# Kernel tuning notes

Measured on AMD Instinct MI355X. Metric: run time of the kernel, lower is better.

Reference implementation:

```python
import jax, jax.numpy as jnp
import numpy as np
from jax import lax

T = 512
CHUNK = 64
H = W = 28
C = 4
D_MODEL = H * W * C  # 3136
D_HIDDEN = 512
ALPHA = 0.9
ETA0 = 0.1
P = 2.0
EPS = 1e-6


def setup_inputs() -> dict:
    key = jax.random.key(0)
    ks = jax.random.split(key, 8)
    x = jax.random.normal(ks[0], (T, C, H, W), dtype=jnp.float32)
    conv_k_w = jax.random.normal(ks[1], (3, 3, C, C), dtype=jnp.float32) / 6.0  # lecun-ish: fan_in=36
    conv_v_w = jax.random.normal(ks[2], (3, 3, C, C), dtype=jnp.float32) / 6.0
    conv_k_b = jnp.zeros((C,), jnp.float32)
    conv_v_b = jnp.zeros((C,), jnp.float32)
    rms_k_scale = jnp.ones((C,), jnp.float32)
    rms_v_scale = jnp.ones((C,), jnp.float32)
    W1 = jax.random.normal(ks[3], (D_MODEL, D_HIDDEN), dtype=jnp.float32) / np.sqrt(D_MODEL).astype(np.float32)
    b1 = jnp.zeros((D_HIDDEN,), jnp.float32)
    W2 = jax.random.normal(ks[4], (D_HIDDEN, D_MODEL), dtype=jnp.float32) / np.sqrt(D_HIDDEN).astype(np.float32)
    b2 = jnp.zeros((D_MODEL,), jnp.float32)
    return {"x": x, "conv_k_w": conv_k_w, "conv_k_b": conv_k_b,
            "conv_v_w": conv_v_w, "conv_v_b": conv_v_b,
            "rms_k_scale": rms_k_scale, "rms_v_scale": rms_v_scale,
            "W1": W1, "b1": b1, "W2": W2, "b2": b2}


def _conv(x_nhwc, w, b):
    y = lax.conv_general_dilated(x_nhwc, w, window_strides=(1, 1), padding='SAME',
                                 dimension_numbers=('NHWC', 'HWIO', 'NHWC'))
    return y + b


def _rmsnorm(z, scale):
    inv = lax.rsqrt(jnp.mean(z * z, axis=-1, keepdims=True) + EPS)
    return z * inv * scale


def _mlp(params, k):
    w1, bb1, w2, bb2 = params
    return jax.nn.gelu(k @ w1 + bb1) @ w2 + bb2


def reference(x, conv_k_w, conv_k_b, conv_v_w, conv_v_b, rms_k_scale, rms_v_scale, W1, b1, W2, b2):
    t = x.shape[0]
    xh = jnp.transpose(x, (0, 2, 3, 1))  # [T,H,W,C]
    nk = _rmsnorm(_conv(xh, conv_k_w, conv_k_b), rms_k_scale).reshape(t, -1)  # [T, D_MODEL]
    nv = _rmsnorm(_conv(xh, conv_v_w, conv_v_b), rms_v_scale).reshape(t, -1)

    params0 = (W1, b1, W2, b2)

    def loss_per_token(params, k, v):
        pred = _mlp(params, k)
        return jnp.sum(jnp.abs(pred - v) ** P)

    etas = ETA0 * ALPHA ** jnp.arange(CHUNK, dtype=jnp.float32)
    betas = ALPHA ** jnp.arange(CHUNK, dtype=jnp.float32)
    weights = etas * (betas[-1] / betas)  # [CHUNK]

    n_chunks = t // CHUNK
    Kc = nk.reshape(n_chunks, CHUNK, D_MODEL)
    Vc = nv.reshape(n_chunks, CHUNK, D_MODEL)

    def chunk_body(params, kv):
        K, V = kv
        # per-token parameter grads: leaves have leading CHUNK axis
        grads = jax.vmap(jax.grad(loss_per_token), in_axes=(None, 0, 0))(params, K, V)
        new_params = jax.tree.map(
            lambda p, g: p - jnp.tensordot(weights, g, axes=((0,), (0,))), params, grads)
        Y = _mlp(new_params, K)  # recall on keys with updated fast weights
        return new_params, Y

    _, Y_chunks = lax.scan(chunk_body, params0, (Kc, Vc))
    Y = Y_chunks.reshape(t, D_MODEL)
    return Y.reshape(t, C, H, W)
```

## Files before the change

kernel.cpp:

```cpp
#include <hip/hip_runtime.h>
#include <math.h>

#define DM 3136
#define DH 512

typedef __attribute__((ext_vector_type(8))) short bf16x8;
typedef __attribute__((ext_vector_type(4))) float f32x4;

__device__ __forceinline__ ushort f2bf(float f) {
  union { float f; unsigned u; } v; v.f = f;
  unsigned r = v.u + 0x7FFFu + ((v.u >> 16) & 1u);
  return (ushort)(r >> 16);
}

#define MICRO_4x4 \
    acc[0][0] += a.x*b.x; acc[0][1] += a.x*b.y; acc[0][2] += a.x*b.z; acc[0][3] += a.x*b.w; \
    acc[1][0] += a.y*b.x; acc[1][1] += a.y*b.y; acc[1][2] += a.y*b.z; acc[1][3] += a.y*b.w; \
    acc[2][0] += a.z*b.x; acc[2][1] += a.z*b.y; acc[2][2] += a.z*b.z; acc[2][3] += a.z*b.w; \
    acc[3][0] += a.w*b.x; acc[3][1] += a.w*b.y; acc[3][2] += a.w*b.z; acc[3][3] += a.w*b.w;

__device__ __forceinline__ void gelu_both(float xx, float& g, float& gp) {
  const float c = 0.7978845608028654f;
  const float a = 0.044715f;
  float x2 = xx * xx;
  float u = c * (xx + a * xx * x2);
  float t = tanhf(u);
  g  = 0.5f * xx * (1.f + t);
  gp = 0.5f * (1.f + t) + 0.5f * xx * (1.f - t * t) * c * (1.f + 3.f * a * x2);
}
__device__ __forceinline__ float gelu_only(float xx) {
  const float c = 0.7978845608028654f;
  const float a = 0.044715f;
  float u = c * (xx + a * xx * xx * xx);
  return 0.5f * xx * (1.f + tanhf(u));
}

__device__ __forceinline__ void nt64_core(
    const ushort* __restrict__ A, int lda,
    const ushort* __restrict__ B, int ldb,
    int ksteps, f32x4* acc) {
  int lane = threadIdx.x & 63;
  int wv = threadIdx.x >> 6;
  int qr = wv >> 1, qc = wv & 1;
  int lr = lane & 15;
  int lk = (lane >> 4) << 3;
  const ushort* pa0 = A + (size_t)(qr * 32 + lr) * lda + lk;
  const ushort* pa1 = pa0 + (size_t)16 * lda;
  const ushort* pb0 = B + (size_t)(qc * 32 + lr) * ldb + lk;
  const ushort* pb1 = pb0 + (size_t)16 * ldb;
  bf16x8 a0 = *(const bf16x8*)pa0;
  bf16x8 a1 = *(const bf16x8*)pa1;
  bf16x8 b0 = *(const bf16x8*)pb0;
  bf16x8 b1 = *(const bf16x8*)pb1;
  for (int s = 0; s < ksteps; ++s) {
    int sn = (s + 1 < ksteps) ? (s + 1) * 32 : s * 32;
    bf16x8 na0 = *(const bf16x8*)(pa0 + sn);
    bf16x8 na1 = *(const bf16x8*)(pa1 + sn);
    bf16x8 nb0 = *(const bf16x8*)(pb0 + sn);
    bf16x8 nb1 = *(const bf16x8*)(pb1 + sn);
    acc[0] = __builtin_amdgcn_mfma_f32_16x16x32_bf16(a0, b0, acc[0], 0, 0, 0);
    acc[1] = __builtin_amdgcn_mfma_f32_16x16x32_bf16(a0, b1, acc[1], 0, 0, 0);
    acc[2] = __builtin_amdgcn_mfma_f32_16x16x32_bf16(a1, b0, acc[2], 0, 0, 0);
    acc[3] = __builtin_amdgcn_mfma_f32_16x16x32_bf16(a1, b1, acc[3], 0, 0, 0);
    a0 = na0; a1 = na1; b0 = nb0; b1 = nb1;
  }
}

__device__ __forceinline__ void nt64_store(const f32x4* acc, float* __restrict__ dst, int ldc) {
  int lane = threadIdx.x & 63, wv = threadIdx.x >> 6;
  int r0 = (wv >> 1) * 32 + ((lane >> 4) << 2);
  int c0 = (wv & 1) * 32 + (lane & 15);
  #pragma unroll
  for (int r = 0; r < 4; ++r) {
    dst[(size_t)(r0 + r) * ldc + c0]           = acc[0][r];
    dst[(size_t)(r0 + r) * ldc + c0 + 16]      = acc[1][r];
    dst[(size_t)(r0 + r + 16) * ldc + c0]      = acc[2][r];
    dst[(size_t)(r0 + r + 16) * ldc + c0 + 16] = acc[3][r];
  }
}

__global__ __launch_bounds__(256) void conv_rms(
    const float* __restrict__ x,
    const float* __restrict__ wk, const float* __restrict__ bk,
    const float* __restrict__ wv, const float* __restrict__ bv,
    const float* __restrict__ sk, const float* __restrict__ sv,
    const float* __restrict__ W1, ushort* __restrict__ w1tb,
    const float* __restrict__ W2, ushort* __restrict__ W2b0, ushort* __restrict__ W2tb0,
    ushort* __restrict__ nkb, float* __restrict__ nv) {
  __shared__ float smem[4160];
  int tid = threadIdx.x;
  if (blockIdx.x >= 1960) {
    int t = blockIdx.x - 1960;
    int d0 = (t % 49) * 64, h0 = (t / 49) * 64;
    int c = tid & 63, rq = tid >> 6;
    #pragma unroll
    for (int q = 0; q < 16; ++q) {
      int r = q * 4 + rq;
      float v = W2[(size_t)(h0 + r) * DM + d0 + c];
      smem[r * 65 + c] = v;
      W2b0[(size_t)(h0 + r) * DM + d0 + c] = f2bf(v);
    }
    __syncthreads();
    #pragma unroll
    for (int q = 0; q < 16; ++q) {
      int r = q * 4 + rq;
      W2tb0[(size_t)(d0 + r) * DH + h0 + c] = f2bf(smem[c * 65 + r]);
    }
    return;
  }
  if (blockIdx.x >= 1568) {
    int t = blockIdx.x - 1568;
    int d0 = (t % 49) * 64, h0 = (t / 49) * 64;
    int c = tid & 63, rq = tid >> 6;
    #pragma unroll
    for (int q = 0; q < 16; ++q) {
      int r = q * 4 + rq;
      smem[r * 65 + c] = W1[(size_t)(d0 + r) * 512 + h0 + c];
    }
    __syncthreads();
    #pragma unroll
    for (int q = 0; q < 16; ++q) {
      int r = q * 4 + rq;
      w1tb[(size_t)(h0 + r) * 3136 + d0 + c] = f2bf(smem[c * 65 + r]);
    }
    return;
  }
  float* swk = smem;
  float* swv = smem + 144;
  float* sb  = smem + 288;
  if (tid < 144) { swk[tid] = wk[tid]; swv[tid] = wv[tid]; }
  if (tid < 4) {
    sb[tid] = bk[tid]; sb[4 + tid] = bv[tid];
    sb[8 + tid] = sk[tid]; sb[12 + tid] = sv[tid];
  }
  __syncthreads();
  int idx = blockIdx.x * 256 + tid;
  int t = idx / 784, hw = idx - t * 784;
  int h = hw / 28, w = hw - h * 28;
  float ak[4], av[4];
  #pragma unroll
  for (int c = 0; c < 4; ++c) { ak[c] = sb[c]; av[c] = sb[4 + c]; }
  const float* xt = x + (size_t)t * DM;
  for (int kh = 0; kh < 3; ++kh) {
    int ih = h + kh - 1;
    if (ih < 0 || ih >= 28) continue;
    for (int kw = 0; kw < 3; ++kw) {
      int iw = w + kw - 1;
      if (iw < 0 || iw >= 28) continue;
      int base = (kh * 3 + kw) * 16;
      #pragma unroll
      for (int ci = 0; ci < 4; ++ci) {
        float xv = xt[ci * 784 + ih * 28 + iw];
        #pragma unroll
        for (int co = 0; co < 4; ++co) {
          ak[co] += xv * swk[base + ci * 4 + co];
          av[co] += xv * swv[base + ci * 4 + co];
        }
      }
    }
  }
  float mk = (ak[0]*ak[0] + ak[1]*ak[1] + ak[2]*ak[2] + ak[3]*ak[3]) * 0.25f + 1e-6f;
  float mv = (av[0]*av[0] + av[1]*av[1] + av[2]*av[2] + av[3]*av[3]) * 0.25f + 1e-6f;
  float ik = 1.f / sqrtf(mk), iv = 1.f / sqrtf(mv);
  ushort4 ok = { f2bf(ak[0]*ik*sb[8]), f2bf(ak[1]*ik*sb[9]),
                 f2bf(ak[2]*ik*sb[10]), f2bf(ak[3]*ik*sb[11]) };
  float4 ov = { av[0]*iv*sb[12], av[1]*iv*sb[13], av[2]*iv*sb[14], av[3]*iv*sb[15] };
  *(ushort4*)&nkb[(size_t)idx * 4] = ok;
  *(float4*)&nv[(size_t)idx * 4] = ov;
}

__global__ __launch_bounds__(256) void u1_kernel(
    const ushort* __restrict__ nkb, const ushort* __restrict__ w1tb,
    float* __restrict__ KKsl, float* __restrict__ Hb_sl) {
  f32x4 acc[4] = {{0.f,0.f,0.f,0.f},{0.f,0.f,0.f,0.f},{0.f,0.f,0.f,0.f},{0.f,0.f,0.f,0.f}};
  int job = blockIdx.x;
  if (job < 448) {
    int s = job % 7;
    int t = job / 7;
    int m0 = (t >> 3) * 64, n0 = (t & 7) * 64;
    nt64_core(nkb + (size_t)m0 * DM + s * 448, DM, w1tb + (size_t)n0 * DM + s * 448, DM, 14, acc);
    nt64_store(acc, Hb_sl + (size_t)s * 262144 + (size_t)m0 * 512 + n0, 512);
  } else {
    int j2 = job - 448;
    int p = j2 / 7, s = j2 % 7;
    int c = 0;
    while ((c + 1) * (c + 2) / 2 <= p) ++c;
    int j = p - c * (c + 1) / 2;
    nt64_core(nkb + (size_t)c * 64 * DM + s * 448, DM, nkb + (size_t)j * 64 * DM + s * 448, DM, 14, acc);
    nt64_store(acc, KKsl + ((size_t)p * 7 + s) * 4096, 64);
  }
}

__global__ __launch_bounds__(256) void u2_kernel(
    const float* __restrict__ KKsl, const float* __restrict__ Hb_sl,
    float* __restrict__ KKf, float* __restrict__ Hbase,
    const float* __restrict__ b1,
    float* __restrict__ Hh, ushort* __restrict__ Gb, ushort* __restrict__ Gtb,
    float* __restrict__ Gp) {
  int i = blockIdx.x * 256 + threadIdx.x;
  if (i < 147456) {
    int pair = i >> 12, e = i & 4095;
    float s = 0.f;
    #pragma unroll
    for (int t = 0; t < 7; ++t) s += KKsl[((size_t)pair * 7 + t) * 4096 + e];
    KKf[i] = s;
  } else {
    int j = i - 147456;
    float s = 0.f;
    #pragma unroll
    for (int t = 0; t < 7; ++t) s += Hb_sl[(size_t)t * 262144 + j];
    Hbase[j] = s;
    if (j < 32768) {
      Hh[j] = s;
      float g, gp;
      gelu_both(s + b1[j & 511], g, gp);
      Gb[j] = f2bf(g);
      Gtb[(j & 511) * 64 + (j >> 9)] = f2bf(g);
      Gp[j] = gp;
    }
  }
}

__device__ __forceinline__ void hred_body(
    int j, const float* __restrict__ Hb_c, const float* __restrict__ Hcorr, int nsl,
    const float* __restrict__ b1v,
    float* __restrict__ Hh, ushort* __restrict__ Gb, ushort* __restrict__ Gtb,
    float* __restrict__ Gp) {
  float s = Hb_c[j];
  for (int t = 0; t < nsl; ++t) s -= Hcorr[(size_t)t * 32768 + j];
  Hh[j] = s;
  float g, gp;
  gelu_both(s + b1v[j & 511], g, gp);
  Gb[j] = f2bf(g);
  Gtb[(j & 511) * 64 + (j >> 9)] = f2bf(g);
  Gp[j] = gp;
}

__device__ __forceinline__ void hs_corr_job(
    const float* __restrict__ KK, const float* __restrict__ Ewj,
    float* __restrict__ dst, int bx, float* smem) {
  float* As = smem;
  float* Bs = smem + 4096;
  int tid = threadIdx.x;
  int n0 = bx * 64;
  {
    int m = tid >> 2, ib = (tid & 3) * 16;
    #pragma unroll
    for (int q = 0; q < 4; ++q) {
      float4 v = *(const float4*)(KK + m * 64 + ib + q * 4);
      As[(ib + q*4 + 0)*64 + m] = v.x;
      As[(ib + q*4 + 1)*64 + m] = v.y;
      As[(ib + q*4 + 2)*64 + m] = v.z;
      As[(ib + q*4 + 3)*64 + m] = v.w;
    }
    int kr = tid >> 4, nn = (tid & 15) * 4;
    #pragma unroll
    for (int q = 0; q < 4; ++q)
      *(float4*)&Bs[(kr + q*16)*64 + nn] = *(const float4*)(Ewj + (size_t)(kr + q*16) * DH + n0 + nn);
  }
  __syncthreads();
  int tx = tid & 15, ty = tid >> 4;
  float acc[4][4] = {{0.f}};
  #pragma unroll 16
  for (int kk = 0; kk < 64; ++kk) {
    float4 a = *(const float4*)&As[kk*64 + ty * 4];
    float4 b = *(const float4*)&Bs[kk*64 + tx * 4];
    MICRO_4x4
  }
  #pragma unroll
  for (int r = 0; r < 4; ++r) {
    float4 v = { acc[r][0], acc[r][1], acc[r][2], acc[r][3] };
    *(float4*)&dst[(ty*4 + r) * DH + n0 + tx*4] = v;
  }
}

__global__ __launch_bounds__(256) void p4w2_kernel(
    const ushort* __restrict__ Dwb, const ushort* __restrict__ Dwtb,
    const ushort* __restrict__ Gtb, const ushort* __restrict__ W2b_c,
    const float* __restrict__ W2c, float* __restrict__ W2n,
    ushort* __restrict__ W2b_n, ushort* __restrict__ W2tb_n,
    float* __restrict__ Esl) {
  f32x4 acc[4] = {{0.f,0.f,0.f,0.f},{0.f,0.f,0.f,0.f},{0.f,0.f,0.f,0.f},{0.f,0.f,0.f,0.f}};
  int b = blockIdx.x;
  if (b < 56) {
    int s = b % 7, nt = b / 7;
    nt64_core(Dwb + s * 448, DM, W2b_c + (size_t)nt * 64 * DM + s * 448, DM, 14, acc);
    nt64_store(acc, Esl + (size_t)s * 32768 + nt * 64, 512);
  } else {
    int li = b - 56;
    int d0 = (li % 49) * 64, h0 = (li / 49) * 64;
    nt64_core(Gtb + (size_t)h0 * 64, 64, Dwtb + (size_t)d0 * 64, 64, 2, acc);
    int lane = threadIdx.x & 63, wvv = threadIdx.x >> 6;
    int r0 = (wvv >> 1) * 32 + ((lane >> 4) << 2);
    int c0 = (wvv & 1) * 32 + (lane & 15);
    #pragma unroll
    for (int r = 0; r < 4; ++r) {
      #pragma unroll
      for (int p = 0; p < 4; ++p) {
        int h = h0 + r0 + r + ((p >> 1) ? 16 : 0);
        int d = d0 + c0 + ((p & 1) ? 16 : 0);
        size_t off = (size_t)h * DM + d;
        float w = W2c[off] - acc[p][r];
        W2n[off] = w;
        ushort wb = f2bf(w);
        W2b_n[off] = wb;
        W2tb_n[(size_t)d * DH + h] = wb;
      }
    }
  }
}

__global__ __launch_bounds__(256) void g2h_kernel(
    const float* __restrict__ KKf, int ch,
    const float* __restrict__ Esl, const float* __restrict__ GpC,
    const float* __restrict__ Hcur, const float* __restrict__ b1e,
    float* __restrict__ b1o, ushort* __restrict__ G2b,
    float* __restrict__ EwOut, float* __restrict__ Hcorr) {
  __shared__ float smem[8192];
  int blk = blockIdx.x;
  int tid = threadIdx.x;
  int tri = ch * (ch + 1) / 2;
  if (blk < 32) {
    float* KKs = smem;
    float* Ews = smem + 4096;
    float* b1l = smem + 5120;
    const float* KKcc = KKf + (size_t)(tri + ch) * 4096;
    int n0 = blk * 16;
    #pragma unroll
    for (int q = 0; q < 4; ++q) {
      int e4 = q * 256 + tid;
      *(float4*)&KKs[e4 * 4] = *(const float4*)(KKcc + e4 * 4);
    }
    #pragma unroll
    for (int q = 0; q < 4; ++q) {
      int e = q * 256 + tid;
      int i = e >> 4, cc = e & 15;
      size_t off = (size_t)i * 512 + n0 + cc;
      float s = 0.f;
      #pragma unroll
      for (int sl = 0; sl < 7; ++sl) s += Esl[(size_t)sl * 32768 + off];
      Ews[e] = s * GpC[off];
    }
    __syncthreads();
    if (tid < 16) {
      float s = 0.f;
      for (int i = 0; i < 64; ++i) s += Ews[i * 16 + tid];
      b1l[tid] = b1e[n0 + tid] - s;
    }
    __syncthreads();
    #pragma unroll
    for (int q = 0; q < 4; ++q) {
      int e = q * 256 + tid;
      int mrow = e >> 4, cc = e & 15;
      float corr = 0.f;
      #pragma unroll 16
      for (int i = 0; i < 64; ++i) corr += KKs[mrow * 64 + i] * Ews[i * 16 + cc];
      float xx = Hcur[(size_t)mrow * 512 + n0 + cc] - corr + b1l[cc];
      G2b[(size_t)mrow * 512 + n0 + cc] = f2bf(gelu_only(xx));
    }
  } else {
    float* As = smem;
    float* Bs = smem + 4096;
    int bx = blk - 32;
    int n0 = bx * 64;
    #pragma unroll
    for (int q = 0; q < 16; ++q) {
      int e = q * 256 + tid;
      int k = e >> 6, c = e & 63;
      size_t off = (size_t)k * 512 + n0 + c;
      float s = 0.f;
      #pragma unroll
      for (int sl = 0; sl < 7; ++sl) s += Esl[(size_t)sl * 32768 + off];
      float ew = s * GpC[off];
      Bs[k * 64 + c] = ew;
      EwOut[off] = ew;
    }
    {
      const float* KK = KKf + (size_t)((ch + 1) * (ch + 2) / 2 + ch) * 4096;
      int m = tid >> 2, ib = (tid & 3) * 16;
      #pragma unroll
      for (int q = 0; q < 4; ++q) {
        float4 v = *(const float4*)(KK + m * 64 + ib + q * 4);
        As[(ib + q*4 + 0)*64 + m] = v.x;
        As[(ib + q*4 + 1)*64 + m] = v.y;
        As[(ib + q*4 + 2)*64 + m] = v.z;
        As[(ib + q*4 + 3)*64 + m] = v.w;
      }
    }
    __syncthreads();
    if (tid < 64) {
      float s = 0.f;
      for (int k = 0; k < 64; ++k) s += Bs[k * 64 + tid];
      b1o[n0 + tid] = b1e[n0 + tid] - s;
    }
    int tx = tid & 15, ty = tid >> 4;
    float acc[4][4] = {{0.f}};
    #pragma unroll 16
    for (int kk = 0; kk < 64; ++kk) {
      float4 a = *(const float4*)&As[kk*64 + ty * 4];
      float4 b = *(const float4*)&Bs[kk*64 + tx * 4];
      MICRO_4x4
    }
    float* dst = Hcorr + (size_t)ch * 32768;
    #pragma unroll
    for (int r = 0; r < 4; ++r) {
      float4 v = { acc[r][0], acc[r][1], acc[r][2], acc[r][3] };
      *(float4*)&dst[(ty*4 + r) * DH + n0 + tx*4] = v;
    }
  }
}

__global__ __launch_bounds__(256) void p7h_kernel(
    const ushort* __restrict__ G2b, const ushort* __restrict__ W2tb,
    const float* __restrict__ b2n, float* __restrict__ out, int t0,
    const float* __restrict__ Hbase_n, const float* __restrict__ Hcorr, int nsl,
    const float* __restrict__ b1n,
    float* __restrict__ Hh, ushort* __restrict__ Gb_n, ushort* __restrict__ Gtb_n,
    float* __restrict__ Gp) {
  int b = blockIdx.x;
  if (b < 49) {
    f32x4 acc[4] = {{0.f,0.f,0.f,0.f},{0.f,0.f,0.f,0.f},{0.f,0.f,0.f,0.f},{0.f,0.f,0.f,0.f}};
    int n0 = b * 64;
    nt64_core(G2b, 512, W2tb + (size_t)n0 * 512, 512, 16, acc);
    int lane = threadIdx.x & 63, wvv = threadIdx.x >> 6;
    int r0 = (wvv >> 1) * 32 + ((lane >> 4) << 2);
    int c0 = (wvv & 1) * 32 + (lane & 15);
    #pragma unroll
    for (int r = 0; r < 4; ++r) {
      #pragma unroll
      for (int p = 0; p < 4; ++p) {
        int m = r0 + r + ((p >> 1) ? 16 : 0);
        int d = n0 + c0 + ((p & 1) ? 16 : 0);
        out[(size_t)(t0 + m) * DM + d] = acc[p][r] + b2n[d];
      }
    }
  } else {
    int j = (b - 49) * 256 + threadIdx.x;
    hred_body(j, Hbase_n, Hcorr, nsl, b1n, Hh, Gb_n, Gtb_n, Gp);
  }
}

__global__ __launch_bounds__(256) void p3d_kernel(
    const ushort* __restrict__ Gnb, const ushort* __restrict__ W2tb,
    const float* __restrict__ Vn, const float* __restrict__ b2in, float wc2,
    float* __restrict__ b2out, ushort* __restrict__ Dwb, ushort* __restrict__ Dwtb,
    const float* __restrict__ KKf, int ch,
    const float* __restrict__ Ewst, float* __restrict__ Hcorr) {
  __shared__ float smem[8192];
  int blk = blockIdx.x;
  if (blk < 49) {
    f32x4 acc[4] = {{0.f,0.f,0.f,0.f},{0.f,0.f,0.f,0.f},{0.f,0.f,0.f,0.f},{0.f,0.f,0.f,0.f}};
    int n0 = blk * 64;
    nt64_core(Gnb, 512, W2tb + (size_t)n0 * 512, 512, 16, acc);
    int lane = threadIdx.x & 63, wvv = threadIdx.x >> 6;
    int qr = wvv >> 1, qc = wvv & 1;
    int r0 = qr * 32 + ((lane >> 4) << 2);
    int c0 = qc * 32 + (lane & 15);
    float csum[2] = {0.f, 0.f};
    #pragma unroll
    for (int r = 0; r < 4; ++r) {
      #pragma unroll
      for (int p = 0; p < 4; ++p) {
        int m = r0 + r + ((p >> 1) ? 16 : 0);
        int dl = c0 + ((p & 1) ? 16 : 0);
        int d = n0 + dl;
        float dw = wc2 * (acc[p][r] + b2in[d] - Vn[(size_t)m * DM + d]);
        ushort db = f2bf(dw);
        Dwb[(size_t)m * DM + d] = db;
        Dwtb[(size_t)d * 64 + m] = db;
        csum[p & 1] += dw;
      }
    }
    int slot = qr * 4 + ((lane >> 4) & 3);
    smem[(size_t)c0 * 8 + slot] = csum[0];
    smem[(size_t)(c0 + 16) * 8 + slot] = csum[1];
    __syncthreads();
    if (threadIdx.x < 64) {
      float s = 0.f;
      #pragma unroll
      for (int q = 0; q < 8; ++q) s += smem[threadIdx.x * 8 + q];
      b2out[n0 + threadIdx.x] = b2in[n0 + threadIdx.x] - s;
    }
  } else {
    int j2 = blk - 49;
    int j = j2 >> 3, bx = j2 & 7;
    int trin = (ch + 2) * (ch + 3) / 2;
    hs_corr_job(KKf + (size_t)(trin + j) * 4096, Ewst + (size_t)j * 32768,
                Hcorr + (size_t)j * 32768, bx, smem);
  }
}

extern "C" void kernel_launch(void* const* d_in, const int* in_sizes, int n_in,
                              void* d_out, int out_size, void* d_ws, size_t ws_size,
                              hipStream_t stream) {
  const float* x  = (const float*)d_in[0];
  const float* wk = (const float*)d_in[1];
  const float* bk = (const float*)d_in[2];
  const float* wv = (const float*)d_in[3];
  const float* bv = (const float*)d_in[4];
  const float* sk = (const float*)d_in[5];
  const float* sv = (const float*)d_in[6];
  const float* W1 = (const float*)d_in[7];
  const float* b1 = (const float*)d_in[8];
  const float* W2 = (const float*)d_in[9];
  const float* b2 = (const float*)d_in[10];
  float* out = (float*)d_out;
  float* ws  = (float*)d_ws;

  ushort* nkb   = (ushort*)ws;
  ushort* w1tb  = (ushort*)(ws + 802816);
  float* nv     = ws + 1605632;
  float* W2A    = nv + 1605632;
  float* W2B    = W2A + 1605632;
  float* bf_base = W2B + 1605632;
  ushort* W2b0  = (ushort*)bf_base;
  ushort* W2tb0 = (ushort*)(bf_base + 802816);
  ushort* W2bA  = (ushort*)(bf_base + 1605632);
  ushort* W2bB  = (ushort*)(bf_base + 2408448);
  ushort* W2tbA = (ushort*)(bf_base + 3211264);
  ushort* W2tbB = (ushort*)(bf_base + 4014080);
  float* Esl    = bf_base + 4816896;
  float* Hb_sl  = Esl + 229376;
  float* KKsl   = Hb_sl + 1835008;
  float* Hbase  = KKsl + 1032192;
  float* KKf    = Hbase + 262144;
  float* HhA    = KKf + 147456;
  float* HhB    = HhA + 32768;
  float* GpA    = HhB + 32768;
  float* GpB    = GpA + 32768;
  ushort* GbA   = (ushort*)(GpB + 32768);
  ushort* GbB   = (ushort*)(GpB + 49152);
  ushort* GtbA  = (ushort*)(GpB + 65536);
  ushort* GtbB  = (ushort*)(GpB + 81920);
  ushort* G2b   = (ushort*)(GpB + 98304);
  ushort* Dwb   = (ushort*)(GpB + 114688);
  ushort* Dwtb  = (ushort*)(GpB + 215040);
  float* Ewst   = GpB + 315392;
  float* Hcorr  = Ewst + 262144;
  float* b1A    = Hcorr + 229376;
  float* b1B    = b1A + 512;
  float* b2A    = b1B + 512;
  float* b2B    = b2A + 3136;

  float* W2buf[2]   = { W2A, W2B };
  ushort* W2bb[2]   = { W2bA, W2bB };
  ushort* W2tbb[2]  = { W2tbA, W2tbB };
  ushort* Gbb[2]    = { GbA, GbB };
  ushort* Gtbb[2]   = { GtbA, GtbB };
  float* Hhb[2]     = { HhA, HhB };
  float* Gpb[2]     = { GpA, GpB };
  float* b1buf[2]   = { b1A, b1B };
  float* b2buf[2]   = { b2A, b2B };

  float wc2 = 2.0f * (float)(0.1 * pow(0.9, 63.0));

  conv_rms<<<2352, 256, 0, stream>>>(x, wk, bk, wv, bv, sk, sv,
                                     W1, w1tb, W2, W2b0, W2tb0, nkb, nv);
  u1_kernel<<<700, 256, 0, stream>>>(nkb, w1tb, KKsl, Hb_sl);
  u2_kernel<<<1600, 256, 0, stream>>>(KKsl, Hb_sl, KKf, Hbase, b1, HhA, GbA, GtbA, GpA);
  p3d_kernel<<<49, 256, 0, stream>>>(GbA, W2tb0, nv, b2, wc2, b2A, Dwb, Dwtb,
                                     KKf, 0, Ewst, Hcorr);

  for (int ch = 0; ch < 8; ++ch) {
    const float* b1e  = ch ? b1buf[(ch - 1) & 1] : b1;
    const float* W2c  = ch ? W2buf[(ch - 1) & 1] : W2;
    const ushort* W2b_c = ch ? W2bb[(ch - 1) & 1] : W2b0;

    p4w2_kernel<<<448, 256, 0, stream>>>(
        Dwb, Dwtb, Gtbb[ch & 1], W2b_c, W2c,
        W2buf[ch & 1], W2bb[ch & 1], W2tbb[ch & 1], Esl);
    g2h_kernel<<<32 + (ch < 7 ? 8 : 0), 256, 0, stream>>>(
        KKf, ch, Esl, Gpb[ch & 1], Hhb[ch & 1], b1e, b1buf[ch & 1],
        G2b, Ewst + (size_t)ch * 32768, Hcorr);
    p7h_kernel<<<49 + (ch < 7 ? 128 : 0), 256, 0, stream>>>(
        G2b, W2tbb[ch & 1], b2buf[ch & 1], out, ch * 64,
        Hbase + (size_t)((ch + 1) & 7) * 32768, Hcorr, ch + 1, b1buf[ch & 1],
        Hhb[(ch + 1) & 1], Gbb[(ch + 1) & 1], Gtbb[(ch + 1) & 1], Gpb[(ch + 1) & 1]);
    if (ch < 7) {
      int gF = 49 + (ch < 6 ? 8 * (ch + 1) : 0);
      p3d_kernel<<<gF, 256, 0, stream>>>(
          Gbb[(ch + 1) & 1], W2tbb[ch & 1], nv + (size_t)(ch + 1) * 200704,
          b2buf[ch & 1], wc2, b2buf[(ch + 1) & 1], Dwb, Dwtb,
          KKf, ch, Ewst, Hcorr);
    }
  }
}
```

Baseline: 418.2 us.

## Replace explicit W2 updates with low-rank correction terms against the original W2

Stops materializing the updated W2 matrix (fp32 plus two bf16 copies) every chunk. W2 is now kept implicitly as the original W2 minus a sum of low-rank G^T·Dw products, and all Dw and G histories are stored. Predictions and error backprop are rebuilt from the original W2 plus small 64x64 Gram-style corrections (DD, -G·G^T). The per-chunk kernels are regrouped into four stages, and the hidden-state recompute is folded into the g2h-like kernel. The goal is to remove the large 512x3136 read-modify-write per chunk, at the cost of correction work that grows with the chunk index and extra rounding from bf16 correction matrices.

```diff
diff --git a/kernel.cpp b/kernel.cpp
--- a/kernel.cpp
+++ b/kernel.cpp
@@ -11,6 +11,10 @@
   union { float f; unsigned u; } v; v.f = f;
   unsigned r = v.u + 0x7FFFu + ((v.u >> 16) & 1u);
   return (ushort)(r >> 16);
+}
+__device__ __forceinline__ float bf2f(ushort u) {
+  union { float f; unsigned u; } v; v.u = ((unsigned)u) << 16;
+  return v.f;
 }
 
 #define MICRO_4x4 \
@@ -79,6 +83,57 @@
   }
 }
 
+__device__ __forceinline__ void store_neg_gg(const f32x4* acc, ushort* __restrict__ dst) {
+  int lane = threadIdx.x & 63, wv = threadIdx.x >> 6;
+  int r0 = (wv >> 1) * 32 + ((lane >> 4) << 2);
+  int c0 = (wv & 1) * 32 + (lane & 15);
+  #pragma unroll
+  for (int r = 0; r < 4; ++r) {
+    #pragma unroll
+    for (int p = 0; p < 4; ++p) {
+      int m = r0 + r + ((p >> 1) ? 16 : 0);
+      int n = c0 + ((p & 1) ? 16 : 0);
+      dst[m * 64 + n] = f2bf(-acc[p][r]);
+    }
+  }
+}
+
+__device__ __forceinline__ void dw_epilogue(
+    const f32x4* acc, int n0, const float* __restrict__ Vn,
+    const float* __restrict__ b2in, float wc2,
+    ushort* __restrict__ Dwb_o, ushort* __restrict__ Dwt_o,
+    float* __restrict__ b2out, float* smem) {
+  int lane = threadIdx.x & 63, wvv = threadIdx.x >> 6;
+  int qr = wvv >> 1, qc = wvv & 1;
+  int r0 = qr * 32 + ((lane >> 4) << 2);
+  int c0 = qc * 32 + (lane & 15);
+  float csum[2] = {0.f, 0.f};
+  #pragma unroll
+  for (int r = 0; r < 4; ++r) {
+    #pragma unroll
+    for (int p = 0; p < 4; ++p) {
+      int m = r0 + r + ((p >> 1) ? 16 : 0);
+      int dl = c0 + ((p & 1) ? 16 : 0);
+      int d = n0 + dl;
+      float dw = wc2 * (acc[p][r] + b2in[d] - Vn[(size_t)m * DM + d]);
+      ushort db = f2bf(dw);
+      Dwb_o[(size_t)m * DM + d] = db;
+      Dwt_o[(size_t)d * 64 + m] = db;
+      csum[p & 1] += dw;
+    }
+  }
+  int slot = qr * 4 + ((lane >> 4) & 3);
+  smem[(size_t)c0 * 8 + slot] = csum[0];
+  smem[(size_t)(c0 + 16) * 8 + slot] = csum[1];
+  __syncthreads();
+  if (threadIdx.x < 64) {
+    float s = 0.f;
+    #pragma unroll
+    for (int q = 0; q < 8; ++q) s += smem[threadIdx.x * 8 + q];
+    b2out[n0 + threadIdx.x] = b2in[n0 + threadIdx.x] - s;
+  }
+}
+
 __global__ __launch_bounds__(256) void conv_rms(
     const float* __restrict__ x,
     const float* __restrict__ wk, const float* __restrict__ bk,
@@ -221,21 +276,6 @@
   }
 }
 
-__device__ __forceinline__ void hred_body(
-    int j, const float* __restrict__ Hb_c, const float* __restrict__ Hcorr, int nsl,
-    const float* __restrict__ b1v,
-    float* __restrict__ Hh, ushort* __restrict__ Gb, ushort* __restrict__ Gtb,
-    float* __restrict__ Gp) {
-  float s = Hb_c[j];
-  for (int t = 0; t < nsl; ++t) s -= Hcorr[(size_t)t * 32768 + j];
-  Hh[j] = s;
-  float g, gp;
-  gelu_both(s + b1v[j & 511], g, gp);
-  Gb[j] = f2bf(g);
-  Gtb[(j & 511) * 64 + (j >> 9)] = f2bf(g);
-  Gp[j] = gp;
-}
-
 __device__ __forceinline__ void hs_corr_job(
     const float* __restrict__ KK, const float* __restrict__ Ewj,
     float* __restrict__ dst, int bx, float* smem) {
@@ -274,154 +314,176 @@
   }
 }
 
-__global__ __launch_bounds__(256) void p4w2_kernel(
-    const ushort* __restrict__ Dwb, const ushort* __restrict__ Dwtb,
-    const ushort* __restrict__ Gtb, const ushort* __restrict__ W2b_c,
-    const float* __restrict__ W2c, float* __restrict__ W2n,
-    ushort* __restrict__ W2b_n, ushort* __restrict__ W2tb_n,
-    float* __restrict__ Esl) {
+__global__ __launch_bounds__(256) void pred0_kernel(
+    const ushort* __restrict__ Gb0, const ushort* __restrict__ W2tb0,
+    const float* __restrict__ V, const float* __restrict__ b2in, float wc2,
+    float* __restrict__ b2out, ushort* __restrict__ Dwb_o, ushort* __restrict__ Dwt_o) {
+  __shared__ float smem[512];
+  f32x4 acc[4] = {{0.f,0.f,0.f,0.f},{0.f,0.f,0.f,0.f},{0.f,0.f,0.f,0.f},{0.f,0.f,0.f,0.f}};
+  int n0 = blockIdx.x * 64;
+  nt64_core(Gb0, 512, W2tb0 + (size_t)n0 * 512, 512, 16, acc);
+  dw_epilogue(acc, n0, V, b2in, wc2, Dwb_o, Dwt_o, b2out, smem);
+}
+
+__global__ __launch_bounds__(256) void kA_kernel(
+    const ushort* __restrict__ Dwb_ch, const ushort* __restrict__ W2b0,
+    const ushort* __restrict__ Dwb_all, float* __restrict__ Esl,
+    float* __restrict__ DD) {
   f32x4 acc[4] = {{0.f,0.f,0.f,0.f},{0.f,0.f,0.f,0.f},{0.f,0.f,0.f,0.f},{0.f,0.f,0.f,0.f}};
   int b = blockIdx.x;
   if (b < 56) {
     int s = b % 7, nt = b / 7;
-    nt64_core(Dwb + s * 448, DM, W2b_c + (size_t)nt * 64 * DM + s * 448, DM, 14, acc);
+    nt64_core(Dwb_ch + s * 448, DM, W2b0 + (size_t)nt * 64 * DM + s * 448, DM, 14, acc);
     nt64_store(acc, Esl + (size_t)s * 32768 + nt * 64, 512);
   } else {
-    int li = b - 56;
-    int d0 = (li % 49) * 64, h0 = (li / 49) * 64;
-    nt64_core(Gtb + (size_t)h0 * 64, 64, Dwtb + (size_t)d0 * 64, 64, 2, acc);
-    int lane = threadIdx.x & 63, wvv = threadIdx.x >> 6;
-    int r0 = (wvv >> 1) * 32 + ((lane >> 4) << 2);
-    int c0 = (wvv & 1) * 32 + (lane & 15);
-    #pragma unroll
-    for (int r = 0; r < 4; ++r) {
+    int j = b - 56;
+    nt64_core(Dwb_ch, DM, Dwb_all + (size_t)j * 200704, DM, 98, acc);
+    nt64_store(acc, DD + (size_t)j * 4096, 64);
+  }
+}
+
+__global__ __launch_bounds__(256) void kB_kernel(
+    const float* __restrict__ KKf, int ch,
+    const float* __restrict__ Esl, const float* __restrict__ DD,
+    const ushort* __restrict__ Gtb_all, const float* __restrict__ GpC,
+    const float* __restrict__ Hcur, const float* __restrict__ b1e,
+    float* __restrict__ b1o, ushort* __restrict__ G2b, float* __restrict__ EwOut,
+    const float* __restrict__ Hcorr, const float* __restrict__ Hbase_n,
+    float* __restrict__ HhN, ushort* __restrict__ GbN,
+    ushort* __restrict__ GtbN, float* __restrict__ GpN) {
+  __shared__ float sKK[4096];
+  __shared__ float sKK2[4096];
+  __shared__ float sDD[4096];
+  __shared__ float sG[1024];
+  __shared__ float sEw[1024];
+  __shared__ float b1l[16];
+  int tid = threadIdx.x;
+  int n0 = blockIdx.x * 16;
+  int tri = ch * (ch + 1) / 2;
+  {
+    const float* KKcc = KKf + (size_t)(tri + ch) * 4096;
+    #pragma unroll
+    for (int q = 0; q < 4; ++q)
+      ((float4*)sKK)[q * 256 + tid] = ((const float4*)KKcc)[q * 256 + tid];
+    if (ch < 7) {
+      const float* KKn = KKf + (size_t)((ch + 1) * (ch + 2) / 2 + ch) * 4096;
       #pragma unroll
-      for (int p = 0; p < 4; ++p) {
-        int h = h0 + r0 + r + ((p >> 1) ? 16 : 0);
-        int d = d0 + c0 + ((p & 1) ? 16 : 0);
-        size_t off = (size_t)h * DM + d;
-        float w = W2c[off] - acc[p][r];
-        W2n[off] = w;
-        ushort wb = f2bf(w);
-        W2b_n[off] = wb;
-        W2tb_n[(size_t)d * DH + h] = wb;
-      }
-    }
-  }
-}
-
-__global__ __launch_bounds__(256) void g2h_kernel(
-    const float* __restrict__ KKf, int ch,
-    const float* __restrict__ Esl, const float* __restrict__ GpC,
-    const float* __restrict__ Hcur, const float* __restrict__ b1e,
-    float* __restrict__ b1o, ushort* __restrict__ G2b,
-    float* __restrict__ EwOut, float* __restrict__ Hcorr) {
-  __shared__ float smem[8192];
-  int blk = blockIdx.x;
-  int tid = threadIdx.x;
-  int tri = ch * (ch + 1) / 2;
-  if (blk < 32) {
-    float* KKs = smem;
-    float* Ews = smem + 4096;
-    float* b1l = smem + 5120;
-    const float* KKcc = KKf + (size_t)(tri + ch) * 4096;
-    int n0 = blk * 16;
-    #pragma unroll
-    for (int q = 0; q < 4; ++q) {
-      int e4 = q * 256 + tid;
-      *(float4*)&KKs[e4 * 4] = *(const float4*)(KKcc + e4 * 4);
-    }
+      for (int q = 0; q < 4; ++q)
+        ((float4*)sKK2)[q * 256 + tid] = ((const float4*)KKn)[q * 256 + tid];
+    }
+  }
+  float eDel[4] = {0.f, 0.f, 0.f, 0.f};
+  for (int j = 0; j < ch; ++j) {
+    __syncthreads();
+    const float* DDj = DD + (size_t)j * 4096;
+    #pragma unroll
+    for (int q = 0; q < 4; ++q)
+      ((float4*)sDD)[q * 256 + tid] = ((const float4*)DDj)[q * 256 + tid];
+    const ushort* Gt = Gtb_all + (size_t)j * 32768 + (size_t)n0 * 64;
     #pragma unroll
     for (int q = 0; q < 4; ++q) {
       int e = q * 256 + tid;
-      int i = e >> 4, cc = e & 15;
-      size_t off = (size_t)i * 512 + n0 + cc;
-      float s = 0.f;
-      #pragma unroll
-      for (int sl = 0; sl < 7; ++sl) s += Esl[(size_t)sl * 32768 + off];
-      Ews[e] = s * GpC[off];
-    }
-    __syncthreads();
-    if (tid < 16) {
-      float s = 0.f;
-      for (int i = 0; i < 64; ++i) s += Ews[i * 16 + tid];
-      b1l[tid] = b1e[n0 + tid] - s;
+      sG[e] = bf2f(Gt[e]);
     }
     __syncthreads();
     #pragma unroll
     for (int q = 0; q < 4; ++q) {
       int e = q * 256 + tid;
-      int mrow = e >> 4, cc = e & 15;
-      float corr = 0.f;
+      int m = e >> 4, c = e & 15;
+      float s = 0.f;
       #pragma unroll 16
-      for (int i = 0; i < 64; ++i) corr += KKs[mrow * 64 + i] * Ews[i * 16 + cc];
-      float xx = Hcur[(size_t)mrow * 512 + n0 + cc] - corr + b1l[cc];
-      G2b[(size_t)mrow * 512 + n0 + cc] = f2bf(gelu_only(xx));
-    }
+      for (int n = 0; n < 64; ++n) s += sDD[m * 64 + n] * sG[c * 64 + n];
+      eDel[q] += s;
+    }
+  }
+  __syncthreads();
+  #pragma unroll
+  for (int q = 0; q < 4; ++q) {
+    int e = q * 256 + tid;
+    int m = e >> 4, c = e & 15;
+    size_t off = (size_t)m * 512 + n0 + c;
+    float s = 0.f;
+    #pragma unroll
+    for (int sl = 0; sl < 7; ++sl) s += Esl[(size_t)sl * 32768 + off];
+    float ew = (s - eDel[q]) * GpC[off];
+    sEw[m * 16 + c] = ew;
+    EwOut[off] = ew;
+  }
+  __syncthreads();
+  if (tid < 16) {
+    float s = 0.f;
+    for (int i = 0; i < 64; ++i) s += sEw[i * 16 + tid];
+    float nb = b1e[n0 + tid] - s;
+    b1l[tid] = nb;
+    b1o[n0 + tid] = nb;
+  }
+  __syncthreads();
+  #pragma unroll
+  for (int q = 0; q < 4; ++q) {
+    int e = q * 256 + tid;
+    int m = e >> 4, c = e & 15;
+    float corr = 0.f;
+    #pragma unroll 16
+    for (int i = 0; i < 64; ++i) corr += sKK[m * 64 + i] * sEw[i * 16 + c];
+    float xx = Hcur[(size_t)m * 512 + n0 + c] - corr + b1l[c];
+    G2b[(size_t)m * 512 + n0 + c] = f2bf(gelu_only(xx));
+  }
+  if (ch < 7) {
+    #pragma unroll
+    for (int q = 0; q < 4; ++q) {
+      int e = q * 256 + tid;
+      int m = e >> 4, c = e & 15;
+      size_t off = (size_t)m * 512 + n0 + c;
+      float corrH = 0.f;
+      #pragma unroll 16
+      for (int i = 0; i < 64; ++i) corrH += sKK2[m * 64 + i] * sEw[i * 16 + c];
+      float s = Hbase_n[off] - corrH;
+      for (int j = 0; j < ch; ++j) s -= Hcorr[(size_t)j * 32768 + off];
+      HhN[off] = s;
+      float g, gp;
+      gelu_both(s + b1l[c], g, gp);
+      GbN[off] = f2bf(g);
+      GtbN[(size_t)(n0 + c) * 64 + m] = f2bf(g);
+      GpN[off] = gp;
+    }
+  }
+}
+
+__global__ __launch_bounds__(256) void kC_kernel(
+    const ushort* __restrict__ G2b, const ushort* __restrict__ Gb_all,
+    const ushort* __restrict__ GbNext, int ch,
+    ushort* __restrict__ mGG2, ushort* __restrict__ mGG) {
+  f32x4 acc[4] = {{0.f,0.f,0.f,0.f},{0.f,0.f,0.f,0.f},{0.f,0.f,0.f,0.f},{0.f,0.f,0.f,0.f}};
+  int b = blockIdx.x;
+  if (b <= ch) {
+    nt64_core(G2b, 512, Gb_all + (size_t)b * 32768, 512, 16, acc);
+    store_neg_gg(acc, mGG2 + (size_t)b * 4096);
   } else {
-    float* As = smem;
-    float* Bs = smem + 4096;
-    int bx = blk - 32;
-    int n0 = bx * 64;
-    #pragma unroll
-    for (int q = 0; q < 16; ++q) {
-      int e = q * 256 + tid;
-      int k = e >> 6, c = e & 63;
-      size_t off = (size_t)k * 512 + n0 + c;
-      float s = 0.f;
-      #pragma unroll
-      for (int sl = 0; sl < 7; ++sl) s += Esl[(size_t)sl * 32768 + off];
-      float ew = s * GpC[off];
-      Bs[k * 64 + c] = ew;
-      EwOut[off] = ew;
-    }
-    {
-      const float* KK = KKf + (size_t)((ch + 1) * (ch + 2) / 2 + ch) * 4096;
-      int m = tid >> 2, ib = (tid & 3) * 16;
-      #pragma unroll
-      for (int q = 0; q < 4; ++q) {
-        float4 v = *(const float4*)(KK + m * 64 + ib + q * 4);
-        As[(ib + q*4 + 0)*64 + m] = v.x;
-        As[(ib + q*4 + 1)*64 + m] = v.y;
-        As[(ib + q*4 + 2)*64 + m] = v.z;
-        As[(ib + q*4 + 3)*64 + m] = v.w;
-      }
-    }
-    __syncthreads();
-    if (tid < 64) {
-      float s = 0.f;
-      for (int k = 0; k < 64; ++k) s += Bs[k * 64 + tid];
-      b1o[n0 + tid] = b1e[n0 + tid] - s;
-    }
-    int tx = tid & 15, ty = tid >> 4;
-    float acc[4][4] = {{0.f}};
-    #pragma unroll 16
-    for (int kk = 0; kk < 64; ++kk) {
-      float4 a = *(const float4*)&As[kk*64 + ty * 4];
-      float4 b = *(const float4*)&Bs[kk*64 + tx * 4];
-      MICRO_4x4
-    }
-    float* dst = Hcorr + (size_t)ch * 32768;
-    #pragma unroll
-    for (int r = 0; r < 4; ++r) {
-      float4 v = { acc[r][0], acc[r][1], acc[r][2], acc[r][3] };
-      *(float4*)&dst[(ty*4 + r) * DH + n0 + tx*4] = v;
-    }
-  }
-}
-
-__global__ __launch_bounds__(256) void p7h_kernel(
-    const ushort* __restrict__ G2b, const ushort* __restrict__ W2tb,
+    int j = b - (ch + 1);
+    nt64_core(GbNext, 512, Gb_all + (size_t)j * 32768, 512, 16, acc);
+    store_neg_gg(acc, mGG + (size_t)j * 4096);
+  }
+}
+
+__global__ __launch_bounds__(256) void kD_kernel(
+    const ushort* __restrict__ G2b, const ushort* __restrict__ W2tb0,
+    const ushort* __restrict__ mGG2, const ushort* __restrict__ mGG,
+    const ushort* __restrict__ Dwt_all, int ch,
     const float* __restrict__ b2n, float* __restrict__ out, int t0,
-    const float* __restrict__ Hbase_n, const float* __restrict__ Hcorr, int nsl,
-    const float* __restrict__ b1n,
-    float* __restrict__ Hh, ushort* __restrict__ Gb_n, ushort* __restrict__ Gtb_n,
-    float* __restrict__ Gp) {
+    const ushort* __restrict__ GbNext, const float* __restrict__ Vn,
+    float wc2, float* __restrict__ b2out,
+    ushort* __restrict__ Dwb_o, ushort* __restrict__ Dwt_o,
+    const float* __restrict__ KKf, const float* __restrict__ Ewst,
+    float* __restrict__ Hcorr) {
+  __shared__ float smem[8192];
   int b = blockIdx.x;
   if (b < 49) {
     f32x4 acc[4] = {{0.f,0.f,0.f,0.f},{0.f,0.f,0.f,0.f},{0.f,0.f,0.f,0.f},{0.f,0.f,0.f,0.f}};
     int n0 = b * 64;
-    nt64_core(G2b, 512, W2tb + (size_t)n0 * 512, 512, 16, acc);
+    nt64_core(G2b, 512, W2tb0 + (size_t)n0 * 512, 512, 16, acc);
+    for (int j = 0; j <= ch; ++j)
+      nt64_core(mGG2 + (size_t)j * 4096, 64,
+                Dwt_all + (size_t)j * 200704 + (size_t)n0 * 64, 64, 2, acc);
     int lane = threadIdx.x & 63, wvv = threadIdx.x >> 6;
     int r0 = (wvv >> 1) * 32 + ((lane >> 4) << 2);
     int c0 = (wvv & 1) * 32 + (lane & 15);
@@ -434,55 +496,16 @@
         out[(size_t)(t0 + m) * DM + d] = acc[p][r] + b2n[d];
       }
     }
+  } else if (ch < 7 && b < 98) {
+    f32x4 acc[4] = {{0.f,0.f,0.f,0.f},{0.f,0.f,0.f,0.f},{0.f,0.f,0.f,0.f},{0.f,0.f,0.f,0.f}};
+    int n0 = (b - 49) * 64;
+    nt64_core(GbNext, 512, W2tb0 + (size_t)n0 * 512, 512, 16, acc);
+    for (int j = 0; j <= ch; ++j)
+      nt64_core(mGG + (size_t)j * 4096, 64,
+                Dwt_all + (size_t)j * 200704 + (size_t)n0 * 64, 64, 2, acc);
+    dw_epilogue(acc, n0, Vn, b2n, wc2, Dwb_o, Dwt_o, b2out, smem);
   } else {
-    int j = (b - 49) * 256 + threadIdx.x;
-    hred_body(j, Hbase_n, Hcorr, nsl, b1n, Hh, Gb_n, Gtb_n, Gp);
-  }
-}
-
-__global__ __launch_bounds__(256) void p3d_kernel(
-    const ushort* __restrict__ Gnb, const ushort* __restrict__ W2tb,
-    const float* __restrict__ Vn, const float* __restrict__ b2in, float wc2,
-    float* __restrict__ b2out, ushort* __restrict__ Dwb, ushort* __restrict__ Dwtb,
-    const float* __restrict__ KKf, int ch,
-    const float* __restrict__ Ewst, float* __restrict__ Hcorr) {
-  __shared__ float smem[8192];
-  int blk = blockIdx.x;
-  if (blk < 49) {
-    f32x4 acc[4] = {{0.f,0.f,0.f,0.f},{0.f,0.f,0.f,0.f},{0.f,0.f,0.f,0.f},{0.f,0.f,0.f,0.f}};
-    int n0 = blk * 64;
-    nt64_core(Gnb, 512, W2tb + (size_t)n0 * 512, 512, 16, acc);
-    int lane = threadIdx.x & 63, wvv = threadIdx.x >> 6;
-    int qr = wvv >> 1, qc = wvv & 1;
-    int r0 = qr * 32 + ((lane >> 4) << 2);
-    int c0 = qc * 32 + (lane & 15);
-    float csum[2] = {0.f, 0.f};
-    #pragma unroll
-    for (int r = 0; r < 4; ++r) {
-      #pragma unroll
-      for (int p = 0; p < 4; ++p) {
-        int m = r0 + r + ((p >> 1) ? 16 : 0);
-        int dl = c0 + ((p & 1) ? 16 : 0);
-        int d = n0 + dl;
-        float dw = wc2 * (acc[p][r] + b2in[d] - Vn[(size_t)m * DM + d]);
-        ushort db = f2bf(dw);
-        Dwb[(size_t)m * DM + d] = db;
-        Dwtb[(size_t)d * 64 + m] = db;
-        csum[p & 1] += dw;
-      }
-    }
-    int slot = qr * 4 + ((lane >> 4) & 3);
-    smem[(size_t)c0 * 8 + slot] = csum[0];
-    smem[(size_t)(c0 + 16) * 8 + slot] = csum[1];
-    __syncthreads();
-    if (threadIdx.x < 64) {
-      float s = 0.f;
-      #pragma unroll
-      for (int q = 0; q < 8; ++q) s += smem[threadIdx.x * 8 + q];
-      b2out[n0 + threadIdx.x] = b2in[n0 + threadIdx.x] - s;
-    }
-  } else {
-    int j2 = blk - 49;
+    int j2 = b - (ch < 7 ? 98 : 49);
     int j = j2 >> 3, bx = j2 & 7;
     int trin = (ch + 2) * (ch + 3) / 2;
     hs_corr_job(KKf + (size_t)(trin + j) * 4096, Ewst + (size_t)j * 32768,
@@ -507,81 +530,75 @@
   float* out = (float*)d_out;
   float* ws  = (float*)d_ws;
 
-  ushort* nkb   = (ushort*)ws;
-  ushort* w1tb  = (ushort*)(ws + 802816);
-  float* nv     = ws + 1605632;
-  float* W2A    = nv + 1605632;
-  float* W2B    = W2A + 1605632;
-  float* bf_base = W2B + 1605632;
-  ushort* W2b0  = (ushort*)bf_base;
-  ushort* W2tb0 = (ushort*)(bf_base + 802816);
-  ushort* W2bA  = (ushort*)(bf_base + 1605632);
-  ushort* W2bB  = (ushort*)(bf_base + 2408448);
-  ushort* W2tbA = (ushort*)(bf_base + 3211264);
-  ushort* W2tbB = (ushort*)(bf_base + 4014080);
-  float* Esl    = bf_base + 4816896;
-  float* Hb_sl  = Esl + 229376;
-  float* KKsl   = Hb_sl + 1835008;
-  float* Hbase  = KKsl + 1032192;
-  float* KKf    = Hbase + 262144;
-  float* HhA    = KKf + 147456;
-  float* HhB    = HhA + 32768;
-  float* GpA    = HhB + 32768;
-  float* GpB    = GpA + 32768;
-  ushort* GbA   = (ushort*)(GpB + 32768);
-  ushort* GbB   = (ushort*)(GpB + 49152);
-  ushort* GtbA  = (ushort*)(GpB + 65536);
-  ushort* GtbB  = (ushort*)(GpB + 81920);
-  ushort* G2b   = (ushort*)(GpB + 98304);
-  ushort* Dwb   = (ushort*)(GpB + 114688);
-  ushort* Dwtb  = (ushort*)(GpB + 215040);
-  float* Ewst   = GpB + 315392;
-  float* Hcorr  = Ewst + 262144;
-  float* b1A    = Hcorr + 229376;
-  float* b1B    = b1A + 512;
-  float* b2A    = b1B + 512;
-  float* b2B    = b2A + 3136;
-
-  float* W2buf[2]   = { W2A, W2B };
-  ushort* W2bb[2]   = { W2bA, W2bB };
-  ushort* W2tbb[2]  = { W2tbA, W2tbB };
-  ushort* Gbb[2]    = { GbA, GbB };
-  ushort* Gtbb[2]   = { GtbA, GtbB };
-  float* Hhb[2]     = { HhA, HhB };
-  float* Gpb[2]     = { GpA, GpB };
-  float* b1buf[2]   = { b1A, b1B };
-  float* b2buf[2]   = { b2A, b2B };
+  ushort* nkb     = (ushort*)ws;
+  ushort* w1tb    = (ushort*)(ws + 802816);
+  float* nv       = ws + 1605632;
+  ushort* W2b0    = (ushort*)(ws + 3211264);
+  ushort* W2tb0   = (ushort*)(ws + 4014080);
+  float* Esl      = ws + 4816896;
+  float* Hb_sl    = Esl + 229376;
+  float* KKsl     = Hb_sl + 1835008;
+  float* Hbase    = KKsl + 1032192;
+  float* KKf      = Hbase + 262144;
+  float* HhA      = KKf + 147456;
+  float* HhB      = HhA + 32768;
+  float* GpA      = HhB + 32768;
+  float* GpB      = GpA + 32768;
+  ushort* Gb_all  = (ushort*)(GpB + 32768);
+  ushort* Gtb_all = (ushort*)(GpB + 163840);
+  ushort* G2b     = (ushort*)(GpB + 294912);
+  ushort* Dwb_all = (ushort*)(GpB + 311296);
+  ushort* Dwt_all = (ushort*)(GpB + 1114112);
+  float* DD       = GpB + 1916928;
+  ushort* mGG2    = (ushort*)(GpB + 1949696);
+  ushort* mGG     = (ushort*)(GpB + 1966080);
+  float* Ewst     = GpB + 1982464;
+  float* Hcorr    = Ewst + 262144;
+  float* b1A      = Hcorr + 229376;
+  float* b1B      = b1A + 512;
+  float* b2A      = b1B + 512;
+  float* b2B      = b2A + 3136;
+
+  float* Hhb[2]   = { HhA, HhB };
+  float* Gpb[2]   = { GpA, GpB };
+  float* b1buf[2] = { b1A, b1B };
+  float* b2buf[2] = { b2A, b2B };
 
   float wc2 = 2.0f * (float)(0.1 * pow(0.9, 63.0));
 
   conv_rms<<<2352, 256, 0, stream>>>(x, wk, bk, wv, bv, sk, sv,
                                      W1, w1tb, W2, W2b0, W2tb0, nkb, nv);
   u1_kernel<<<700, 256, 0, stream>>>(nkb, w1tb, KKsl, Hb_sl);
-  u2_kernel<<<1600, 256, 0, stream>>>(KKsl, Hb_sl, KKf, Hbase, b1, HhA, GbA, GtbA, GpA);
-  p3d_kernel<<<49, 256, 0, stream>>>(GbA, W2tb0, nv, b2, wc2, b2A, Dwb, Dwtb,
-                                     KKf, 0, Ewst, Hcorr);
+  u2_kernel<<<1600, 256, 0, stream>>>(KKsl, Hb_sl, KKf, Hbase, b1,
+                                      HhA, Gb_all, Gtb_all, GpA);
+  pred0_kernel<<<49, 256, 0, stream>>>(Gb_all, W2tb0, nv, b2, wc2, b2A,
+                                       Dwb_all, Dwt_all);
 
   for (int ch = 0; ch < 8; ++ch) {
-    const float* b1e  = ch ? b1buf[(ch - 1) & 1] : b1;
-    const float* W2c  = ch ? W2buf[(ch - 1) & 1] : W2;
-    const ushort* W2b_c = ch ? W2bb[(ch - 1) & 1] : W2b0;
-
-    p4w2_kernel<<<448, 256, 0, stream>>>(
-        Dwb, Dwtb, Gtbb[ch & 1], W2b_c, W2c,
-        W2buf[ch & 1], W2bb[ch & 1], W2tbb[ch & 1], Esl);
-    g2h_kernel<<<32 + (ch < 7 ? 8 : 0), 256, 0, stream>>>(
-        KKf, ch, Esl, Gpb[ch & 1], Hhb[ch & 1], b1e, b1buf[ch & 1],
-        G2b, Ewst + (size_t)ch * 32768, Hcorr);
-    p7h_kernel<<<49 + (ch < 7 ? 128 : 0), 256, 0, stream>>>(
-        G2b, W2tbb[ch & 1], b2buf[ch & 1], out, ch * 64,
-        Hbase + (size_t)((ch + 1) & 7) * 32768, Hcorr, ch + 1, b1buf[ch & 1],
-        Hhb[(ch + 1) & 1], Gbb[(ch + 1) & 1], Gtbb[(ch + 1) & 1], Gpb[(ch + 1) & 1]);
-    if (ch < 7) {
-      int gF = 49 + (ch < 6 ? 8 * (ch + 1) : 0);
-      p3d_kernel<<<gF, 256, 0, stream>>>(
-          Gbb[(ch + 1) & 1], W2tbb[ch & 1], nv + (size_t)(ch + 1) * 200704,
-          b2buf[ch & 1], wc2, b2buf[(ch + 1) & 1], Dwb, Dwtb,
-          KKf, ch, Ewst, Hcorr);
-    }
-  }
-}
+    const float* b1e = ch ? b1buf[(ch - 1) & 1] : b1;
+
+    kA_kernel<<<56 + ch, 256, 0, stream>>>(
+        Dwb_all + (size_t)ch * 200704, W2b0, Dwb_all, Esl, DD);
+    kB_kernel<<<32, 256, 0, stream>>>(
+        KKf, ch, Esl, DD, Gtb_all, Gpb[ch & 1], Hhb[ch & 1], b1e,
+        b1buf[ch & 1], G2b, Ewst + (size_t)ch * 32768,
+        Hcorr, Hbase + (size_t)((ch + 1) & 7) * 32768,
+        Hhb[(ch + 1) & 1],
+        Gb_all + (size_t)((ch + 1) & 7) * 32768,
+        Gtb_all + (size_t)((ch + 1) & 7) * 32768,
+        Gpb[(ch + 1) & 1]);
+    int gC = (ch < 7) ? (2 * ch + 2) : (ch + 1);
+    kC_kernel<<<gC, 256, 0, stream>>>(
+        G2b, Gb_all, Gb_all + (size_t)((ch + 1) & 7) * 32768, ch, mGG2, mGG);
+    int gD = 49 + (ch < 7 ? 49 : 0) + (ch < 6 ? 8 * (ch + 1) : 0);
+    kD_kernel<<<gD, 256, 0, stream>>>(
+        G2b, W2tb0, mGG2, mGG, Dwt_all, ch,
+        b2buf[ch & 1], out, ch * 64,
+        Gb_all + (size_t)((ch + 1) & 7) * 32768,
+        nv + (size_t)((ch + 1) & 7) * 200704,
+        wc2, b2buf[(ch + 1) & 1],
+        Dwb_all + (size_t)((ch + 1) & 7) * 200704,
+        Dwt_all + (size_t)((ch + 1) & 7) * 200704,
+        KKf, Ewst, Hcorr);
+  }
+}
```

New measurement: 967.5 us. 2.31x slower.
